# Performance work log

Hardware: AMD Instinct MI355X
Metric: run time of the kernel (lower is better)

## Reference

```python
import jax, jax.numpy as jnp
import numpy as np

HQ, HKV, DK, DV = 8, 4, 128, 128
WIDTH, CLIP, MAXPOS = 16, 5.0, 2048
EPS = 1e-5

def rms_bn(x, g, ch_axis):
    # EMA_RMSBatchNorm (eval with batch stats): per-channel RMS over all other dims
    axes = tuple(i for i in range(x.ndim) if i != ch_axis)
    ms = jnp.mean(jnp.square(x), axis=axes, keepdims=True)
    shape = [1] * x.ndim; shape[ch_axis] = g.shape[0]
    return x * jax.lax.rsqrt(ms + EPS) * g.reshape(shape)

def ln(x, g, b):
    m = jnp.mean(x, -1, keepdims=True)
    v = jnp.mean(jnp.square(x - m), -1, keepdims=True)
    return (x - m) * jax.lax.rsqrt(v + EPS) * g + b

def rope(x):
    # x: [B,S,H,C], custom AlphaGenome frequency schedule
    B, S, H, C = x.shape
    nf = C // 2
    pos = jnp.arange(S, dtype=x.dtype)
    lin = jnp.arange(nf, dtype=x.dtype)
    end = max(MAXPOS - nf + 1.0, 1.0)
    geom = jnp.exp(jnp.linspace(0.0, np.log(end), nf).astype(x.dtype))
    inv_freq = 1.0 / (lin + geom)
    theta = jnp.repeat(pos[:, None] * inv_freq, 2, axis=-1)[None, :, None, :]  # [1,S,1,C]
    x_rot = jnp.stack([-x[..., 1::2], x[..., ::2]], axis=-1).reshape(x.shape)
    return x * jnp.cos(theta) + x_rot * jnp.sin(theta)

def _forward(x, pair_x, ab_bn_g, ab_fc_w, bn1_g, wq, wk, wv, qn_g, qn_b, kn_g, kn_b,
             vn_g, vn_b, wo, bo, bn2_g, mbn1_g, w1, b1, w2, b2, mbn2_g):
    B, S, C = x.shape
    # --- AttentionBias from pair representation ---
    pb = rms_bn(pair_x, ab_bn_g, 3)
    pb = jax.nn.gelu(pb, approximate=False)
    pb = jnp.einsum('bijc,gc->bijg', pb, ab_fc_w)          # [B,Sp,Sp,group]
    pb = jnp.repeat(jnp.repeat(pb, WIDTH, axis=1), WIDTH, axis=2)  # upsample to [B,S,S,group]
    bias = jnp.repeat(jnp.transpose(pb, (0, 3, 1, 2)), HKV, axis=1)  # [B,HQ,S,S]
    # --- GQA attention ---
    xn = rms_bn(x, bn1_g, 2)
    q = ln((xn @ wq.T).reshape(B, S, HQ, DK), qn_g, qn_b)
    k = ln((xn @ wk.T).reshape(B, S, HKV, DK), kn_g, kn_b)
    v = ln((xn @ wv.T).reshape(B, S, HKV, DV), vn_g, vn_b)
    q = rope(q); k = rope(k)
    rep = HQ // HKV
    k = jnp.tile(k, (1, 1, rep, 1))  # torch .repeat: [k0..k3, k0..k3]
    v = jnp.tile(v, (1, 1, rep, 1))
    logits = jnp.einsum('bshd,bThd->bhsT', q, k) / np.float32(np.sqrt(DK)) + bias
    logits = jnp.tanh(logits / CLIP) * CLIP
    attn = jax.nn.softmax(logits, axis=-1)
    y = jnp.einsum('bhsT,bThd->bshd', attn, v)
    # faithful to original: permute then reshape (layout scramble preserved)
    y = jnp.transpose(y, (0, 2, 1, 3)).reshape(B, S, HQ * DV)
    x = x + rms_bn(y @ wo.T + bo, bn2_g, 2)
    # --- MLP block ---
    h = jax.nn.relu(rms_bn(x, mbn1_g, 2) @ w1.T + b1)
    x = x + rms_bn(h @ w2.T + b2, mbn2_g, 2)
    return x, pair_x

def setup_inputs() -> dict:
    key = jax.random.key(0)
    ks = jax.random.split(key, 10)
    B, S, C, SP, PC = 2, 2048, 768, 128, 128
    n = lambda k, sh: jax.random.normal(k, sh, jnp.float32) * 0.02
    d = {}
    d['x'] = jax.random.normal(ks[0], (B, S, C), jnp.float32)
    d['pair_x'] = jax.random.normal(ks[1], (B, SP, SP, PC), jnp.float32)
    d['ab_bn_g'] = jnp.ones((PC,), jnp.float32)
    d['ab_fc_w'] = n(ks[2], (HQ // HKV, PC))
    d['bn1_g'] = jnp.ones((C,), jnp.float32)
    d['wq'] = n(ks[3], (HQ * DK, C))
    d['wk'] = n(ks[4], (HKV * DK, C))
    d['wv'] = n(ks[5], (HKV * DV, C))
    d['qn_g'] = jnp.ones((DK,), jnp.float32); d['qn_b'] = jnp.zeros((DK,), jnp.float32)
    d['kn_g'] = jnp.ones((DK,), jnp.float32); d['kn_b'] = jnp.zeros((DK,), jnp.float32)
    d['vn_g'] = jnp.ones((DV,), jnp.float32); d['vn_b'] = jnp.zeros((DV,), jnp.float32)
    d['wo'] = n(ks[6], (C, HQ * DV)); d['bo'] = jnp.zeros((C,), jnp.float32)
    d['bn2_g'] = jnp.ones((C,), jnp.float32)
    d['mbn1_g'] = jnp.ones((C,), jnp.float32)
    d['w1'] = n(ks[7], (2 * C, C)); d['b1'] = jnp.zeros((2 * C,), jnp.float32)
    d['w2'] = n(ks[8], (C, 2 * C)); d['b2'] = jnp.zeros((C,), jnp.float32)
    d['mbn2_g'] = jnp.ones((C,), jnp.float32)
    return d

def reference(x, pair_x, ab_bn_g, ab_fc_w, bn1_g, wq, wk, wv, qn_g, qn_b, kn_g, kn_b,
              vn_g, vn_b, wo, bo, bn2_g, mbn1_g, w1, b1, w2, b2, mbn2_g):
    return _forward(x, pair_x, ab_bn_g, ab_fc_w, bn1_g, wq, wk, wv, qn_g, qn_b, kn_g,
                    kn_b, vn_g, vn_b, wo, bo, bn2_g, mbn1_g, w1, b1, w2, b2, mbn2_g)
```

## Files before the change

kernel.cpp:

```cpp
#include <hip/hip_runtime.h>
#include <math.h>

#define EPS 1e-5f

typedef __attribute__((ext_vector_type(8))) short short8;
typedef __attribute__((ext_vector_type(4))) float f32x4;

namespace {

constexpr int Bn = 2, Sn = 2048, Cn = 768;
constexpr float INV_BS = 1.0f / 4096.0f;
constexpr float INV_PAIR = 1.0f / 32768.0f;
constexpr float LOG2E = 1.4426950408889634f;

__device__ __forceinline__ ushort f2bf(float f) {
  uint u = __float_as_uint(f);
  u = (u + 0x7fffu + ((u >> 16) & 1u)) >> 16;
  return (ushort)u;
}
__device__ __forceinline__ float bf2f(ushort u) {
  return __uint_as_float(((uint)u) << 16);
}
__device__ __forceinline__ uint cvt_pk_bf16(float lo, float hi) {
  uint r;
  asm("v_cvt_pk_bf16_f32 %0, %1, %2" : "=v"(r) : "v"(lo), "v"(hi));
  return r;
}
__device__ __forceinline__ void gl16(const ushort* g, ushort* l) {
  __builtin_amdgcn_global_load_lds(
      (const __attribute__((address_space(1))) unsigned int*)(unsigned long long)(size_t)g,
      (__attribute__((address_space(3))) unsigned int*)(unsigned int)(size_t)l, 16, 0, 0);
}

#define KSW(r, c) ((((r) * 128) + (c)) ^ (((r) & 7) * 8))
#define VTW(d, t) ((((d) * 64) + (t)) ^ (((d) & 7) * 8))
#define PSW2(w, q, c) ((w) * 2048 + ((((q) * 64) + (c)) ^ (((q) & 7) * 8)))

__global__ void castall_k(const float* __restrict__ wq, const float* __restrict__ wk,
                          const float* __restrict__ wv, const float* __restrict__ wo,
                          const float* __restrict__ w1, const float* __restrict__ w2,
                          ushort* __restrict__ dst) {
  int u = blockIdx.x * 256 + threadIdx.x;
  const float* src; int local;
  if (u < 98304)       { src = wq; local = u; }
  else if (u < 147456) { src = wk; local = u - 98304; }
  else if (u < 196608) { src = wv; local = u - 147456; }
  else if (u < 294912) { src = wo; local = u - 196608; }
  else if (u < 442368) { src = w1; local = u - 294912; }
  else                 { src = w2; local = u - 442368; }
  int i = local * 8;
  float4 a = *(const float4*)&src[i];
  float4 b = *(const float4*)&src[i + 4];
  union { short8 s8; ushort us[8]; } o;
  o.us[0] = f2bf(a.x); o.us[1] = f2bf(a.y); o.us[2] = f2bf(a.z); o.us[3] = f2bf(a.w);
  o.us[4] = f2bf(b.x); o.us[5] = f2bf(b.y); o.us[6] = f2bf(b.z); o.us[7] = f2bf(b.w);
  *(short8*)&dst[u * 8] = o.s8;
}

__global__ void rope_tab_k(float2* __restrict__ tab) {
  int idx = blockIdx.x * 256 + threadIdx.x;
  int s = idx >> 6, i = idx & 63;
  const float kGeo = logf(1985.0f) * (1.0f / 63.0f);
  float inv = 1.0f / ((float)i + expf((float)i * kGeo));
  float th = (float)s * inv;
  tab[idx] = make_float2(cosf(th), sinf(th));
}

__global__ void scale_cast_k(const float* __restrict__ a, const float* __restrict__ sums,
                             const float* __restrict__ g, ushort* __restrict__ o) {
  int idx = blockIdx.x * 256 + threadIdx.x;
  int c0 = (idx % 96) * 8;
  int base = idx * 8;
  float4 v0 = *(const float4*)&a[base];
  float4 v1 = *(const float4*)&a[base + 4];
  union { short8 s8; ushort us[8]; } r;
  float vv[8] = {v0.x, v0.y, v0.z, v0.w, v1.x, v1.y, v1.z, v1.w};
#pragma unroll
  for (int j = 0; j < 8; ++j) {
    float sc = rsqrtf(sums[c0 + j] * INV_BS + EPS) * g[c0 + j];
    r.us[j] = f2bf(vv[j] * sc);
  }
  *(short8*)&o[base] = r.s8;
}

__global__ void pair_sumsq_k(const float* __restrict__ p, float* __restrict__ out) {
  int r0 = blockIdx.x * 128;
  float acc = 0.f;
  for (int r = 0; r < 128; ++r) {
    float v = p[(size_t)(r0 + r) * 128 + threadIdx.x];
    acc += v * v;
  }
  atomicAdd(&out[threadIdx.x], acc);
}

__global__ void ch_sumsq768_k(const float* __restrict__ a, float* __restrict__ out) {
  int r0 = blockIdx.x * 16;
  int c = threadIdx.x;
  float acc = 0.f;
  for (int r = 0; r < 16; ++r) {
    float v = a[(size_t)(r0 + r) * 768 + c];
    acc += v * v;
  }
  atomicAdd(&out[c], acc);
}

__global__ __launch_bounds__(256) void pair_bias_k(
    const float* __restrict__ p, const float* __restrict__ ps,
    const float* __restrict__ g, const float* __restrict__ w,
    float* __restrict__ pb2, float* __restrict__ pcopy) {
  const int tid = threadIdx.x;
  const int lane32 = tid & 31;
  const int sub = tid >> 5;
  const int c0 = lane32 * 4;
  float4 gv = *(const float4*)&g[c0];
  float4 psv = *(const float4*)&ps[c0];
  float4 w0 = *(const float4*)&w[c0];
  float4 w1v = *(const float4*)&w[128 + c0];
  float sc[4] = {rsqrtf(psv.x * INV_PAIR + EPS) * gv.x,
                 rsqrtf(psv.y * INV_PAIR + EPS) * gv.y,
                 rsqrtf(psv.z * INV_PAIR + EPS) * gv.z,
                 rsqrtf(psv.w * INV_PAIR + EPS) * gv.w};
  float wa[4] = {w0.x, w0.y, w0.z, w0.w};
  float wb[4] = {w1v.x, w1v.y, w1v.z, w1v.w};
#pragma unroll
  for (int it = 0; it < 4; ++it) {
    int row = blockIdx.x * 32 + it * 8 + sub;
    float4 v = *(const float4*)&p[(size_t)row * 128 + c0];
    *(float4*)&pcopy[(size_t)row * 128 + c0] = v;
    float vv[4] = {v.x, v.y, v.z, v.w};
    float a0 = 0.f, a1 = 0.f;
#pragma unroll
    for (int j = 0; j < 4; ++j) {
      float x = vv[j] * sc[j];
      float ge = 0.5f * x * (1.f + erff(x * 0.70710678118654752f));
      a0 += ge * wa[j];
      a1 += ge * wb[j];
    }
#pragma unroll
    for (int o = 1; o <= 16; o <<= 1) {
      a0 += __shfl_xor(a0, o);
      a1 += __shfl_xor(a1, o);
    }
    if (lane32 == 0) {
      pb2[(size_t)row * 2 + 0] = a0 * (0.4f * LOG2E);
      pb2[(size_t)row * 2 + 1] = a1 * (0.4f * LOG2E);
    }
  }
}

template <bool RELU, bool OUT_BF16>
__global__ __launch_bounds__(256) void gemm_bf16_k(
    const ushort* __restrict__ A, const ushort* __restrict__ B,
    void* __restrict__ Cv, int M, int N, int K,
    const float* __restrict__ bias) {
  __shared__ __align__(16) ushort As[128 * 64];
  __shared__ __align__(16) ushort Bs[128 * 64];
  const int m0 = blockIdx.y * 128, n0 = blockIdx.x * 128;
  const int tid = threadIdx.x;
  const int lane = tid & 63;
  const int wid = tid >> 6;
  const int l15 = lane & 15, l4 = lane >> 4;
  const int wm = (wid >> 1) * 64, wn = (wid & 1) * 64;
  const ushort* asrc[4]; const ushort* bsrc[4];
  ushort* adst[4]; ushort* bdst[4];
#pragma unroll
  for (int u = 0; u < 4; ++u) {
    int ci = u * 256 + tid;
    int r = ci >> 3, s = ci & 7, g = s ^ (r & 7);
    asrc[u] = A + (size_t)(m0 + r) * K + g * 8;
    bsrc[u] = B + (size_t)(n0 + r) * K + g * 8;
    adst[u] = &As[(u * 256 + wid * 64) * 8];
    bdst[u] = &Bs[(u * 256 + wid * 64) * 8];
  }
  f32x4 acc[4][4];
#pragma unroll
  for (int i = 0; i < 4; ++i)
#pragma unroll
    for (int j = 0; j < 4; ++j) acc[i][j] = (f32x4){0.f, 0.f, 0.f, 0.f};
  for (int k0 = 0; k0 < K; k0 += 64) {
#pragma unroll
    for (int u = 0; u < 4; ++u) {
      gl16(asrc[u] + k0, adst[u]);
      gl16(bsrc[u] + k0, bdst[u]);
    }
    __syncthreads();
#pragma unroll
    for (int ks = 0; ks < 2; ++ks) {
      const int sw = ((ks * 4 + l4) ^ (l15 & 7)) * 8;
      short8 af[4], bf[4];
#pragma unroll
      for (int i = 0; i < 4; ++i) af[i] = *(const short8*)&As[(wm + i * 16 + l15) * 64 + sw];
#pragma unroll
      for (int j = 0; j < 4; ++j) bf[j] = *(const short8*)&Bs[(wn + j * 16 + l15) * 64 + sw];
#pragma unroll
      for (int i = 0; i < 4; ++i)
#pragma unroll
        for (int j = 0; j < 4; ++j)
          acc[i][j] = __builtin_amdgcn_mfma_f32_16x16x32_bf16(af[i], bf[j], acc[i][j], 0, 0, 0);
    }
    __syncthreads();
  }
  float* Cf = (float*)Cv;
  ushort* Cb = (ushort*)Cv;
#pragma unroll
  for (int j = 0; j < 4; ++j) {
    int col = n0 + wn + j * 16 + l15;
    float bv = bias ? bias[col] : 0.f;
#pragma unroll
    for (int i = 0; i < 4; ++i) {
      int row = m0 + wm + i * 16 + l4 * 4;
#pragma unroll
      for (int r = 0; r < 4; ++r) {
        float v = acc[i][j][r] + bv;
        if (RELU) v = fmaxf(v, 0.f);
        if (OUT_BF16) Cb[(size_t)(row + r) * N + col] = f2bf(v);
        else Cf[(size_t)(row + r) * N + col] = v;
      }
    }
  }
}

template <bool SUMSQ>
__global__ __launch_bounds__(256) void gemm64_bf16_k(
    const ushort* __restrict__ A, const ushort* __restrict__ B,
    float* __restrict__ Cf, int M, int N, int K,
    const float* __restrict__ bias, float* __restrict__ ssq) {
  __shared__ __align__(16) ushort As[64 * 64];
  __shared__ __align__(16) ushort Bs[128 * 64];
  const int m0 = blockIdx.y * 64, n0 = blockIdx.x * 128;
  const int tid = threadIdx.x;
  const int lane = tid & 63;
  const int wid = tid >> 6;
  const int l15 = lane & 15, l4 = lane >> 4;
  const int wn = wid * 32;
  const ushort* asrc[2]; ushort* adst[2];
  const ushort* bsrc[4]; ushort* bdst[4];
#pragma unroll
  for (int u = 0; u < 2; ++u) {
    int ci = u * 256 + tid;
    int r = ci >> 3, s = ci & 7, g = s ^ (r & 7);
    asrc[u] = A + (size_t)(m0 + r) * K + g * 8;
    adst[u] = &As[(u * 256 + wid * 64) * 8];
  }
#pragma unroll
  for (int u = 0; u < 4; ++u) {
    int ci = u * 256 + tid;
    int r = ci >> 3, s = ci & 7, g = s ^ (r & 7);
    bsrc[u] = B + (size_t)(n0 + r) * K + g * 8;
    bdst[u] = &Bs[(u * 256 + wid * 64) * 8];
  }
  f32x4 acc[4][2];
#pragma unroll
  for (int i = 0; i < 4; ++i)
#pragma unroll
    for (int j = 0; j < 2; ++j) acc[i][j] = (f32x4){0.f, 0.f, 0.f, 0.f};
  for (int k0 = 0; k0 < K; k0 += 64) {
#pragma unroll
    for (int u = 0; u < 2; ++u) gl16(asrc[u] + k0, adst[u]);
#pragma unroll
    for (int u = 0; u < 4; ++u) gl16(bsrc[u] + k0, bdst[u]);
    __syncthreads();
#pragma unroll
    for (int ks = 0; ks < 2; ++ks) {
      const int sw = ((ks * 4 + l4) ^ (l15 & 7)) * 8;
      short8 af[4], bf[2];
#pragma unroll
      for (int i = 0; i < 4; ++i) af[i] = *(const short8*)&As[(i * 16 + l15) * 64 + sw];
#pragma unroll
      for (int j = 0; j < 2; ++j) bf[j] = *(const short8*)&Bs[(wn + j * 16 + l15) * 64 + sw];
#pragma unroll
      for (int i = 0; i < 4; ++i)
#pragma unroll
        for (int j = 0; j < 2; ++j)
          acc[i][j] = __builtin_amdgcn_mfma_f32_16x16x32_bf16(af[i], bf[j], acc[i][j], 0, 0, 0);
    }
    __syncthreads();
  }
#pragma unroll
  for (int j = 0; j < 2; ++j) {
    int col = n0 + wn + j * 16 + l15;
    float bv = bias ? bias[col] : 0.f;
    float sq = 0.f;
#pragma unroll
    for (int i = 0; i < 4; ++i) {
      int row = m0 + i * 16 + l4 * 4;
#pragma unroll
      for (int r = 0; r < 4; ++r) {
        float v = acc[i][j][r] + bv;
        if (SUMSQ) sq += v * v;
        Cf[(size_t)(row + r) * N + col] = v;
      }
    }
    if (SUMSQ) {
      sq += __shfl_xor(sq, 16);
      sq += __shfl_xor(sq, 32);
      if (l4 == 0) atomicAdd(&ssq[col], sq);
    }
  }
}

__global__ __launch_bounds__(256) void ln_rope_k(
    const float* __restrict__ qkv, const float2* __restrict__ rtab,
    const float* __restrict__ qg, const float* __restrict__ qb,
    const float* __restrict__ kg, const float* __restrict__ kb,
    const float* __restrict__ vg, const float* __restrict__ vb,
    ushort* __restrict__ q_b, ushort* __restrict__ k_b, ushort* __restrict__ v_b) {
  const int half = threadIdx.x >> 7;
  const int tid = threadIdx.x & 127;
  const int bs = blockIdx.x * 2 + half;
  const int slot = blockIdx.y;
  const int s = bs & (Sn - 1);
  const int b = bs >> 11;
  const float* src; const float* g; const float* be; ushort* dst; bool dorope; bool isq = false;
  if (slot < 8) {
    src = qkv + (size_t)bs * 2048 + slot * 128;
    g = qg; be = qb;
    dst = q_b + ((size_t)(b * 8 + slot) * Sn + s) * 128;
    dorope = true; isq = true;
  } else if (slot < 12) {
    int h = slot - 8;
    src = qkv + (size_t)bs * 2048 + 1024 + h * 128;
    g = kg; be = kb;
    dst = k_b + ((size_t)(b * 4 + h) * Sn + s) * 128;
    dorope = true;
  } else {
    int h = slot - 12;
    src = qkv + (size_t)bs * 2048 + 1536 + h * 128;
    g = vg; be = vb;
    dst = v_b + ((size_t)(b * 4 + h) * Sn + s) * 128;
    dorope = false;
  }
  __shared__ float sh[2][128];
  __shared__ float red[2][4];
  float v = src[tid];
  float sum = v;
#pragma unroll
  for (int o = 32; o >= 1; o >>= 1) sum += __shfl_xor(sum, o);
  if ((tid & 63) == 0) red[half][tid >> 6] = sum;
  __syncthreads();
  float mean = (red[half][0] + red[half][1]) * (1.f / 128.f);
  float d = v - mean;
  float s2 = d * d;
#pragma unroll
  for (int o = 32; o >= 1; o >>= 1) s2 += __shfl_xor(s2, o);
  if ((tid & 63) == 0) red[half][2 + (tid >> 6)] = s2;
  __syncthreads();
  float var = (red[half][2] + red[half][3]) * (1.f / 128.f);
  float val = d * rsqrtf(var + EPS) * g[tid] + be[tid];
  if (dorope) {
    sh[half][tid] = val;
    __syncthreads();
    float2 cssn = rtab[(s << 6) | (tid >> 1)];
    float rot = (tid & 1) ? sh[half][tid - 1] : -sh[half][tid + 1];
    val = val * cssn.x + rot * cssn.y;
  }
  if (isq) val *= 0.035355339059327376f * LOG2E;
  dst[tid] = f2bf(val);
}

__global__ __launch_bounds__(256) void vtrans_k(const ushort* __restrict__ vb,
                                                ushort* __restrict__ vtt) {
  __shared__ __align__(16) ushort T[64][136];
  const int hv = blockIdx.y, s0 = blockIdx.x * 64;
  const int tid = threadIdx.x;
  const ushort* src = vb + ((size_t)hv * Sn + s0) * 128;
#pragma unroll
  for (int u = 0; u < 4; ++u) {
    int fi = u * 256 + tid;
    int r = fi >> 4, c = (fi & 15) * 8;
    *(float4*)&T[r][c] = *(const float4*)&src[(size_t)r * 128 + c];
  }
  __syncthreads();
  ushort* dst = vtt + (size_t)hv * 128 * Sn + s0;
#pragma unroll
  for (int u = 0; u < 4; ++u) {
    int fi = u * 256 + tid;
    int d = fi >> 3, t8 = (fi & 7) * 8;
    union { float4 f4; ushort us[8]; } o;
#pragma unroll
    for (int j = 0; j < 8; ++j) o.us[j] = T[t8 + j][d];
    *(float4*)&dst[(size_t)d * Sn + t8] = o.f4;
  }
}

__global__ __launch_bounds__(256, 2) void flash_v13_k(
    const ushort* __restrict__ qb, const ushort* __restrict__ kb,
    const ushort* __restrict__ vtt, const float* __restrict__ pb2,
    ushort* __restrict__ part_y, float* __restrict__ part_l) {
  __shared__ __align__(16) ushort Ks[64 * 128];
  __shared__ __align__(16) ushort Vt[128 * 64];
  __shared__ __align__(16) ushort Ps[4 * 32 * 64];
  const int s0 = blockIdx.x * 128;
  const int bh = blockIdx.y;
  const int half = blockIdx.z;
  const int b = bh >> 3, h = bh & 7;
  const int kv = h & 3, grp = h >> 2;
  const int tid = threadIdx.x;
  const int wid = tid >> 6, lane = tid & 63;
  const int l15 = lane & 15, l4 = lane >> 4;
  const ushort* kbase = kb + (size_t)(b * 4 + kv) * Sn * 128;
  const ushort* vbase = vtt + (size_t)(b * 4 + kv) * 128 * Sn;
  const int qr0 = s0 + wid * 32;
  short8 qf[2][4];
#pragma unroll
  for (int rg = 0; rg < 2; ++rg)
#pragma unroll
    for (int kc = 0; kc < 4; ++kc)
      qf[rg][kc] = *(const short8*)&qb[((size_t)bh * Sn + qr0 + rg * 16 + l15) * 128 + kc * 32 + l4 * 8];
  const ushort* ksrc[4]; const ushort* vsrc[4];
  ushort* kdst[4]; ushort* vdst[4];
#pragma unroll
  for (int u = 0; u < 4; ++u) {
    int ci = u * 256 + tid;
    int kr = ci >> 4, kg = (ci & 15) ^ (kr & 7);
    ksrc[u] = kbase + (size_t)kr * 128 + kg * 8;
    kdst[u] = &Ks[(u * 256 + wid * 64) * 8];
    int vd = ci >> 3, vg = (ci & 7) ^ (vd & 7);
    vsrc[u] = vbase + (size_t)vd * Sn + vg * 8;
    vdst[u] = &Vt[(u * 256 + wid * 64) * 8];
  }
  f32x4 y[2][8];
#pragma unroll
  for (int rg = 0; rg < 2; ++rg)
#pragma unroll
    for (int i = 0; i < 8; ++i) y[rg][i] = (f32x4){0.f, 0.f, 0.f, 0.f};
  float lsum[2] = {0.f, 0.f};
  const float C2 = -10.f * LOG2E;
  const int tbeg = half * 512;
  for (int t0 = tbeg; t0 < tbeg + 512; t0 += 64) {
    __syncthreads();
#pragma unroll
    for (int u = 0; u < 4; ++u) {
      gl16(ksrc[u] + (size_t)t0 * 128, kdst[u]);
      gl16(vsrc[u] + t0, vdst[u]);
    }
    __syncthreads();
    f32x4 acc[2][4];
#pragma unroll
    for (int rg = 0; rg < 2; ++rg)
#pragma unroll
      for (int nb = 0; nb < 4; ++nb) acc[rg][nb] = (f32x4){0.f, 0.f, 0.f, 0.f};
    __builtin_amdgcn_s_setprio(1);
#pragma unroll
    for (int kc = 0; kc < 4; ++kc)
#pragma unroll
      for (int nb = 0; nb < 4; ++nb) {
        short8 kf = *(const short8*)&Ks[KSW(nb * 16 + l15, kc * 32 + l4 * 8)];
        acc[0][nb] = __builtin_amdgcn_mfma_f32_16x16x32_bf16(kf, qf[0][kc], acc[0][nb], 0, 0, 0);
        acc[1][nb] = __builtin_amdgcn_mfma_f32_16x16x32_bf16(kf, qf[1][kc], acc[1][nb], 0, 0, 0);
      }
    __builtin_amdgcn_s_setprio(0);
#pragma unroll
    for (int rg = 0; rg < 2; ++rg)
#pragma unroll
      for (int nb = 0; nb < 4; ++nb) {
        float bias = pb2[(((size_t)b * 128 + (s0 >> 4) + wid * 2 + rg) * 128 + (t0 >> 4) + nb) * 2 + grp];
        float p[4];
#pragma unroll
        for (int r = 0; r < 4; ++r) {
          float e = exp2f(acc[rg][nb][r] + bias);
          p[r] = exp2f(C2 * __builtin_amdgcn_rcpf(e + 1.f));
        }
        lsum[rg] += (p[0] + p[1]) + (p[2] + p[3]);
        uint2 pk;
        pk.x = cvt_pk_bf16(p[0], p[1]);
        pk.y = cvt_pk_bf16(p[2], p[3]);
        *(uint2*)&Ps[PSW2(wid, rg * 16 + l15, nb * 16 + l4 * 4)] = pk;
      }
    __builtin_amdgcn_s_setprio(1);
#pragma unroll
    for (int ks = 0; ks < 2; ++ks) {
      short8 pa0 = *(const short8*)&Ps[PSW2(wid, l15, ks * 32 + l4 * 8)];
      short8 pa1 = *(const short8*)&Ps[PSW2(wid, 16 + l15, ks * 32 + l4 * 8)];
#pragma unroll
      for (int nbd = 0; nbd < 8; ++nbd) {
        short8 vf = *(const short8*)&Vt[VTW(nbd * 16 + l15, ks * 32 + l4 * 8)];
        y[0][nbd] = __builtin_amdgcn_mfma_f32_16x16x32_bf16(pa0, vf, y[0][nbd], 0, 0, 0);
        y[1][nbd] = __builtin_amdgcn_mfma_f32_16x16x32_bf16(pa1, vf, y[1][nbd], 0, 0, 0);
      }
    }
    __builtin_amdgcn_s_setprio(0);
  }
#pragma unroll
  for (int rg = 0; rg < 2; ++rg) {
    float ls = lsum[rg];
    ls += __shfl_xor(ls, 16);
    ls += __shfl_xor(ls, 32);
    if (l4 == 0) part_l[(size_t)(half * 16 + bh) * Sn + qr0 + rg * 16 + l15] = ls;
    ushort* pybase = part_y + ((size_t)(half * 16 + bh) * Sn + qr0 + rg * 16) * 128;
#pragma unroll
    for (int nbd = 0; nbd < 8; ++nbd)
#pragma unroll
      for (int r = 0; r < 4; ++r)
        pybase[(size_t)(l4 * 4 + r) * 128 + nbd * 16 + l15] = f2bf(y[rg][nbd][r]);
  }
}

__global__ void combine_k(const ushort* __restrict__ part_y, const float* __restrict__ part_l,
                          ushort* __restrict__ attn_b) {
  int t = blockIdx.x * 256 + threadIdx.x;
  int row = t >> 4;
  size_t o0 = (size_t)row * 128 + (t & 15) * 8;
  float acc[8] = {};
#pragma unroll
  for (int hf = 0; hf < 4; ++hf) {
    union { short8 s8; ushort us[8]; } u;
    u.s8 = *(const short8*)&part_y[o0 + (size_t)hf * 4194304];
#pragma unroll
    for (int j = 0; j < 8; ++j) acc[j] += bf2f(u.us[j]);
  }
  float rcp = 1.f / (part_l[row] + part_l[row + 32768] + part_l[row + 65536] + part_l[row + 98304]);
  union { short8 s8; ushort us[8]; } o;
#pragma unroll
  for (int j = 0; j < 8; ++j) o.us[j] = f2bf(acc[j] * rcp);
  *(short8*)&attn_b[o0] = o.s8;
}

template <bool SUMSQ>
__global__ void add_scale_k(const float* __restrict__ base, const float* __restrict__ delta,
                            const float* __restrict__ sums, const float* __restrict__ g,
                            float* __restrict__ out, float* __restrict__ ssq) {
  const int c = threadIdx.x;
  const float sc = rsqrtf(sums[c] * INV_BS + EPS) * g[c];
  const int r0 = blockIdx.x * 16;
  float sq = 0.f;
  for (int r = 0; r < 16; ++r) {
    size_t idx = (size_t)(r0 + r) * 768 + c;
    float v = base[idx] + delta[idx] * sc;
    out[idx] = v;
    if (SUMSQ) sq += v * v;
  }
  if (SUMSQ) atomicAdd(&ssq[c], sq);
}

}

extern "C" void kernel_launch(void* const* d_in, const int* in_sizes, int n_in,
                              void* d_out, int out_size, void* d_ws, size_t ws_size,
                              hipStream_t stream) {
  const float* x       = (const float*)d_in[0];
  const float* pair_x  = (const float*)d_in[1];
  const float* ab_bn_g = (const float*)d_in[2];
  const float* ab_fc_w = (const float*)d_in[3];
  const float* bn1_g   = (const float*)d_in[4];
  const float* wq      = (const float*)d_in[5];
  const float* wk      = (const float*)d_in[6];
  const float* wv      = (const float*)d_in[7];
  const float* qn_g    = (const float*)d_in[8];
  const float* qn_b    = (const float*)d_in[9];
  const float* kn_g    = (const float*)d_in[10];
  const float* kn_b    = (const float*)d_in[11];
  const float* vn_g    = (const float*)d_in[12];
  const float* vn_b    = (const float*)d_in[13];
  const float* wo      = (const float*)d_in[14];
  const float* bo      = (const float*)d_in[15];
  const float* bn2_g   = (const float*)d_in[16];
  const float* mbn1_g  = (const float*)d_in[17];
  const float* w1      = (const float*)d_in[18];
  const float* b1      = (const float*)d_in[19];
  const float* w2      = (const float*)d_in[20];
  const float* b2      = (const float*)d_in[21];
  const float* mbn2_g  = (const float*)d_in[22];
  float* out = (float*)d_out;
  float* ws = (float*)d_ws;

  float* ps    = ws + 0;
  float* xs    = ws + 256;
  float* es    = ws + 1024;
  float* x2s   = ws + 2048;
  float* fs    = ws + 3072;
  float* pb2   = ws + 4096;
  ushort* wall_b = (ushort*)(ws + 69632);
  ushort* wo_b = (ushort*)(ws + 856064);
  ushort* w1_b = (ushort*)(ws + 1249280);
  ushort* w2_b = (ushort*)(ws + 1839104);
  ushort* xn_b = (ushort*)(ws + 2428928);
  float* qkvtmp = ws + 4001792;
  ushort* q_b  = (ushort*)(ws + 12390400);
  ushort* k_b  = (ushort*)(ws + 14487552);
  ushort* v_b  = (ushort*)(ws + 15536128);
  float2* rtab = (float2*)(ws + 16584704);
  ushort* v_tt = (ushort*)(ws + 2428928);
  ushort* part_y = (ushort*)(ws + 3477504);
  float* part_l = ws + 11866112;
  ushort* attn_b = (ushort*)(ws + 11997184);
  float* proj  = ws + 3477504;
  float* x2    = ws + 6623232;
  ushort* x2n_b = (ushort*)(ws + 9768960);
  ushort* hbuf_b = (ushort*)(ws + 3477504);
  float* proj2 = ws + 11341824;

  (void)hipMemsetAsync(ws, 0, 4096 * sizeof(float), stream);

  castall_k<<<2304, 256, 0, stream>>>(wq, wk, wv, wo, w1, w2, wall_b);
  rope_tab_k<<<512, 256, 0, stream>>>(rtab);

  pair_sumsq_k<<<256, 128, 0, stream>>>(pair_x, ps);
  pair_bias_k<<<1024, 256, 0, stream>>>(pair_x, ps, ab_bn_g, ab_fc_w, pb2, out + 3145728);
  ch_sumsq768_k<<<256, 768, 0, stream>>>(x, xs);
  scale_cast_k<<<1536, 256, 0, stream>>>(x, xs, bn1_g, xn_b);
  gemm_bf16_k<false, false><<<dim3(16, 32), 256, 0, stream>>>(xn_b, wall_b, qkvtmp, 4096, 2048, 768, nullptr);
  ln_rope_k<<<dim3(2048, 16), 256, 0, stream>>>(qkvtmp, rtab, qn_g, qn_b, kn_g, kn_b,
                                                vn_g, vn_b, q_b, k_b, v_b);
  vtrans_k<<<dim3(32, 8), 256, 0, stream>>>(v_b, v_tt);
  flash_v13_k<<<dim3(16, 16, 4), 256, 0, stream>>>(q_b, k_b, v_tt, pb2, part_y, part_l);
  combine_k<<<2048, 256, 0, stream>>>(part_y, part_l, attn_b);
  gemm64_bf16_k<true><<<dim3(6, 64), 256, 0, stream>>>(attn_b, wo_b, proj, 4096, 768, 1024, bo, es);
  add_scale_k<true><<<256, 768, 0, stream>>>(x, proj, es, bn2_g, x2, x2s);
  scale_cast_k<<<1536, 256, 0, stream>>>(x2, x2s, mbn1_g, x2n_b);
  gemm_bf16_k<true, true><<<dim3(12, 32), 256, 0, stream>>>(x2n_b, w1_b, hbuf_b, 4096, 1536, 768, b1);
  gemm64_bf16_k<true><<<dim3(6, 64), 256, 0, stream>>>(hbuf_b, w2_b, proj2, 4096, 768, 1536, b2, fs);
  add_scale_k<false><<<256, 768, 0, stream>>>(x2, proj2, fs, mbn2_g, out, nullptr);
}
```

Measured before the change: 266.7 us.

## Merge prep kernels into one launch and halve flash-attention KV split count

Four small preparation kernels (weight cast, rope table, pair and x channel sum-of-squares) are folded into a single prep_k launch with block-range dispatch, cutting launch overhead. The flash attention kernel now splits the key range into 2 halves of 1024 instead of 4 quarters of 512, and combine reads 2 partials instead of 4. This shrinks partial-output traffic and combine work, but gives the attention kernel half as many blocks (512), which may lower occupancy and load balance across CUs.

```diff
diff --git a/kernel.cpp b/kernel.cpp
--- a/kernel.cpp
+++ b/kernel.cpp
@@ -36,34 +36,59 @@
 #define VTW(d, t) ((((d) * 64) + (t)) ^ (((d) & 7) * 8))
 #define PSW2(w, q, c) ((w) * 2048 + ((((q) * 64) + (c)) ^ (((q) & 7) * 8)))
 
-__global__ void castall_k(const float* __restrict__ wq, const float* __restrict__ wk,
-                          const float* __restrict__ wv, const float* __restrict__ wo,
-                          const float* __restrict__ w1, const float* __restrict__ w2,
-                          ushort* __restrict__ dst) {
-  int u = blockIdx.x * 256 + threadIdx.x;
-  const float* src; int local;
-  if (u < 98304)       { src = wq; local = u; }
-  else if (u < 147456) { src = wk; local = u - 98304; }
-  else if (u < 196608) { src = wv; local = u - 147456; }
-  else if (u < 294912) { src = wo; local = u - 196608; }
-  else if (u < 442368) { src = w1; local = u - 294912; }
-  else                 { src = w2; local = u - 442368; }
-  int i = local * 8;
-  float4 a = *(const float4*)&src[i];
-  float4 b = *(const float4*)&src[i + 4];
-  union { short8 s8; ushort us[8]; } o;
-  o.us[0] = f2bf(a.x); o.us[1] = f2bf(a.y); o.us[2] = f2bf(a.z); o.us[3] = f2bf(a.w);
-  o.us[4] = f2bf(b.x); o.us[5] = f2bf(b.y); o.us[6] = f2bf(b.z); o.us[7] = f2bf(b.w);
-  *(short8*)&dst[u * 8] = o.s8;
-}
-
-__global__ void rope_tab_k(float2* __restrict__ tab) {
-  int idx = blockIdx.x * 256 + threadIdx.x;
-  int s = idx >> 6, i = idx & 63;
-  const float kGeo = logf(1985.0f) * (1.0f / 63.0f);
-  float inv = 1.0f / ((float)i + expf((float)i * kGeo));
-  float th = (float)s * inv;
-  tab[idx] = make_float2(cosf(th), sinf(th));
+__global__ __launch_bounds__(256) void prep_k(
+    const float* __restrict__ wq, const float* __restrict__ wk,
+    const float* __restrict__ wv, const float* __restrict__ wo,
+    const float* __restrict__ w1, const float* __restrict__ w2,
+    ushort* __restrict__ wdst, float2* __restrict__ rtab,
+    const float* __restrict__ pair, float* __restrict__ ps,
+    const float* __restrict__ x, float* __restrict__ xs) {
+  const int blk = blockIdx.x;
+  const int tid = threadIdx.x;
+  if (blk < 2304) {
+    int u = blk * 256 + tid;
+    const float* src; int local;
+    if (u < 98304)       { src = wq; local = u; }
+    else if (u < 147456) { src = wk; local = u - 98304; }
+    else if (u < 196608) { src = wv; local = u - 147456; }
+    else if (u < 294912) { src = wo; local = u - 196608; }
+    else if (u < 442368) { src = w1; local = u - 294912; }
+    else                 { src = w2; local = u - 442368; }
+    int i = local * 8;
+    float4 a = *(const float4*)&src[i];
+    float4 b = *(const float4*)&src[i + 4];
+    union { short8 s8; ushort us[8]; } o;
+    o.us[0] = f2bf(a.x); o.us[1] = f2bf(a.y); o.us[2] = f2bf(a.z); o.us[3] = f2bf(a.w);
+    o.us[4] = f2bf(b.x); o.us[5] = f2bf(b.y); o.us[6] = f2bf(b.z); o.us[7] = f2bf(b.w);
+    *(short8*)&wdst[u * 8] = o.s8;
+  } else if (blk < 2816) {
+    int idx = (blk - 2304) * 256 + tid;
+    int s = idx >> 6, i = idx & 63;
+    const float kGeo = logf(1985.0f) * (1.0f / 63.0f);
+    float inv = 1.0f / ((float)i + expf((float)i * kGeo));
+    float th = (float)s * inv;
+    rtab[idx] = make_float2(cosf(th), sinf(th));
+  } else if (blk < 2944) {
+    int c = tid & 127;
+    int r0 = (blk - 2816) * 256 + (tid >> 7) * 128;
+    float acc = 0.f;
+    for (int r = 0; r < 128; ++r) {
+      float v = pair[(size_t)(r0 + r) * 128 + c];
+      acc += v * v;
+    }
+    atomicAdd(&ps[c], acc);
+  } else {
+    int r0 = (blk - 2944) * 16;
+    float a0 = 0.f, a1 = 0.f, a2 = 0.f;
+    for (int r = 0; r < 16; ++r) {
+      const float* row = x + (size_t)(r0 + r) * 768;
+      float v0 = row[tid], v1 = row[tid + 256], v2 = row[tid + 512];
+      a0 += v0 * v0; a1 += v1 * v1; a2 += v2 * v2;
+    }
+    atomicAdd(&xs[tid], a0);
+    atomicAdd(&xs[tid + 256], a1);
+    atomicAdd(&xs[tid + 512], a2);
+  }
 }
 
 __global__ void scale_cast_k(const float* __restrict__ a, const float* __restrict__ sums,
@@ -81,16 +106,6 @@
     r.us[j] = f2bf(vv[j] * sc);
   }
   *(short8*)&o[base] = r.s8;
-}
-
-__global__ void pair_sumsq_k(const float* __restrict__ p, float* __restrict__ out) {
-  int r0 = blockIdx.x * 128;
-  float acc = 0.f;
-  for (int r = 0; r < 128; ++r) {
-    float v = p[(size_t)(r0 + r) * 128 + threadIdx.x];
-    acc += v * v;
-  }
-  atomicAdd(&out[threadIdx.x], acc);
 }
 
 __global__ void ch_sumsq768_k(const float* __restrict__ a, float* __restrict__ out) {
@@ -383,7 +398,7 @@
   }
 }
 
-__global__ __launch_bounds__(256, 2) void flash_v13_k(
+__global__ __launch_bounds__(256, 2) void flash_v14_k(
     const ushort* __restrict__ qb, const ushort* __restrict__ kb,
     const ushort* __restrict__ vtt, const float* __restrict__ pb2,
     ushort* __restrict__ part_y, float* __restrict__ part_l) {
@@ -426,8 +441,8 @@
     for (int i = 0; i < 8; ++i) y[rg][i] = (f32x4){0.f, 0.f, 0.f, 0.f};
   float lsum[2] = {0.f, 0.f};
   const float C2 = -10.f * LOG2E;
-  const int tbeg = half * 512;
-  for (int t0 = tbeg; t0 < tbeg + 512; t0 += 64) {
+  const int tbeg = half * 1024;
+  for (int t0 = tbeg; t0 < tbeg + 1024; t0 += 64) {
     __syncthreads();
 #pragma unroll
     for (int u = 0; u < 4; ++u) {
@@ -503,13 +518,13 @@
   size_t o0 = (size_t)row * 128 + (t & 15) * 8;
   float acc[8] = {};
 #pragma unroll
-  for (int hf = 0; hf < 4; ++hf) {
+  for (int hf = 0; hf < 2; ++hf) {
     union { short8 s8; ushort us[8]; } u;
     u.s8 = *(const short8*)&part_y[o0 + (size_t)hf * 4194304];
 #pragma unroll
     for (int j = 0; j < 8; ++j) acc[j] += bf2f(u.us[j]);
   }
-  float rcp = 1.f / (part_l[row] + part_l[row + 32768] + part_l[row + 65536] + part_l[row + 98304]);
+  float rcp = 1.f / (part_l[row] + part_l[row + 32768]);
   union { short8 s8; ushort us[8]; } o;
 #pragma unroll
   for (int j = 0; j < 8; ++j) o.us[j] = f2bf(acc[j] * rcp);
@@ -592,18 +607,15 @@
 
   (void)hipMemsetAsync(ws, 0, 4096 * sizeof(float), stream);
 
-  castall_k<<<2304, 256, 0, stream>>>(wq, wk, wv, wo, w1, w2, wall_b);
-  rope_tab_k<<<512, 256, 0, stream>>>(rtab);
-
-  pair_sumsq_k<<<256, 128, 0, stream>>>(pair_x, ps);
+  prep_k<<<3200, 256, 0, stream>>>(wq, wk, wv, wo, w1, w2, wall_b, rtab,
+                                   pair_x, ps, x, xs);
   pair_bias_k<<<1024, 256, 0, stream>>>(pair_x, ps, ab_bn_g, ab_fc_w, pb2, out + 3145728);
-  ch_sumsq768_k<<<256, 768, 0, stream>>>(x, xs);
   scale_cast_k<<<1536, 256, 0, stream>>>(x, xs, bn1_g, xn_b);
   gemm_bf16_k<false, false><<<dim3(16, 32), 256, 0, stream>>>(xn_b, wall_b, qkvtmp, 4096, 2048, 768, nullptr);
   ln_rope_k<<<dim3(2048, 16), 256, 0, stream>>>(qkvtmp, rtab, qn_g, qn_b, kn_g, kn_b,
                                                 vn_g, vn_b, q_b, k_b, v_b);
   vtrans_k<<<dim3(32, 8), 256, 0, stream>>>(v_b, v_tt);
-  flash_v13_k<<<dim3(16, 16, 4), 256, 0, stream>>>(q_b, k_b, v_tt, pb2, part_y, part_l);
+  flash_v14_k<<<dim3(16, 16, 2), 256, 0, stream>>>(q_b, k_b, v_tt, pb2, part_y, part_l);
   combine_k<<<2048, 256, 0, stream>>>(part_y, part_l, attn_b);
   gemm64_bf16_k<true><<<dim3(6, 64), 256, 0, stream>>>(attn_b, wo_b, proj, 4096, 768, 1024, bo, es);
   add_scale_k<true><<<256, 768, 0, stream>>>(x, proj, es, bn2_g, x2, x2s);
```

After: 254.0 us. -4.8%, faster.
